# Optimization experiments

Hardware: AMD Instinct MI355X
Metric: run time of the kernel (lower is better)

## Reference

```python
import jax, jax.numpy as jnp
import numpy as np

L, B, D, Di, N, H, P, K, M, V = 4, 8, 2048, 4096, 128, 64, 64, 4, 8, 50288
Cch = Di + 2 * N           # conv channels = 4352
Dout = 2 * Di + 2 * N + H  # in_proj out = 8512
EPS = 1e-5


def _rms(x, w):
    return x * jax.lax.rsqrt(jnp.mean(x * x, axis=-1, keepdims=True) + EPS) * w


def setup_inputs() -> dict:
    key = jax.random.key(0)
    ks = jax.random.split(key, 16)
    s = 0.02
    return {
        "input_ids": jax.random.randint(ks[0], (B, 1), 0, V),
        "emb": jax.random.normal(ks[1], (V, D)) * s,
        "in_proj_w": jax.random.normal(ks[2], (L, D, Dout)) * s,
        "conv_w": jax.random.normal(ks[3], (L, Cch, K)) * s,
        "conv_b": jax.random.normal(ks[4], (L, Cch)) * s,
        "A_log": jax.random.normal(ks[5], (L, H)) * 0.5,
        "dt_bias": jax.random.normal(ks[6], (L, H)) * 0.5,
        "D_param": jax.random.normal(ks[7], (L, H)) * 0.5,
        "mixer_norm_w": jnp.ones((L, Di)),
        "out_proj_w": jax.random.normal(ks[8], (L, Di, D)) * s,
        "layer_norm_w": jnp.ones((L, D)),
        "norm_f_w": jnp.ones((D,)),
        "W_mc": jax.random.normal(ks[9], (L, M + 1)).at[:, -1].set(5.0),
        "conv_state": jax.random.normal(ks[10], (L, B, Cch, K)) * 0.1,
        "ssm_state": jax.random.normal(ks[11], (L, B, H, P, N)) * 0.1,
        "cached_states": jax.random.normal(ks[12], (L, B, M, H, P, N)) * 0.1,
    }


def reference(input_ids, emb, in_proj_w, conv_w, conv_b, A_log, dt_bias, D_param,
              mixer_norm_w, out_proj_w, layer_norm_w, norm_f_w, W_mc,
              conv_state, ssm_state, cached_states):
    ids = input_ids[:, 0]              # (B,)
    res = emb[ids]                     # (B, D) token embedding gather
    for l in range(L):
        xn = _rms(res, layer_norm_w[l])
        zxbcdt = xn @ in_proj_w[l]     # (B, Dout)
        z = zxbcdt[:, :Di]
        xBC = zxbcdt[:, Di:Di + Cch]
        dt = zxbcdt[:, Di + Cch:]
        # circular conv-state shift + depthwise conv over kernel dim
        cs = jnp.concatenate([conv_state[l][:, :, 1:], xBC[:, :, None]], axis=-1)
        xBC = jax.nn.silu(jnp.sum(cs * conv_w[l][None], axis=-1) + conv_b[l])
        x, Bm, Cm = xBC[:, :Di], xBC[:, Di:Di + N], xBC[:, Di + N:]
        dt = jax.nn.softplus(dt + dt_bias[l])                 # (B, H)
        dA = jnp.exp(dt * (-jnp.exp(A_log[l])))               # (B, H)
        x = x.reshape(B, H, P)
        dBx = jnp.einsum('bh,bn,bhp->bhpn', dt, Bm, x)        # (B,H,P,N)
        ssm = ssm_state[l] * dA[:, :, None, None] + dBx       # (B,H,P,N)
        # softmax-weighted fusion of cached segment states + current state
        w = jax.nn.softmax(W_mc[l])                           # (M+1,)
        fused = jnp.einsum('bmhpn,m->bhpn', cached_states[l], w[:-1]) + w[-1] * ssm
        y = jnp.einsum('bhpn,bn->bhp', fused, Cm) + D_param[l][None, :, None] * x
        y = y.reshape(B, Di)
        y = _rms(y * jax.nn.silu(z), mixer_norm_w[l])         # gated RMSNorm
        res = res + y @ out_proj_w[l]
    res = _rms(res, norm_f_w)
    logits = res @ emb.T               # tied lm_head
    return logits[:, None, :]          # (B, 1, V)
```

## Files before the change

### kernel.cpp

```cpp
#include <hip/hip_runtime.h>
#include <hip/hip_bf16.h>
#include <math.h>

#define LN 4
#define B_ 8
#define D_ 2048
#define DI 4096
#define N_ 128
#define H_ 64
#define P_ 64
#define K_ 4
#define M_ 8
#define V_ 50288
#define CCH (DI + 2*N_)
#define DOUT (2*DI + 2*N_ + H_)
#define EPSF 1e-5f
#define KT_IN 32
#define KT_OUT 128

typedef float f32x4 __attribute__((ext_vector_type(4)));

__device__ inline float wave_sum(float v) {
  #pragma unroll
  for (int off = 32; off > 0; off >>= 1) v += __shfl_xor(v, off, 64);
  return v;
}

__device__ inline float fold_reduce8(const float a[8], int lane) {
  float t0[4];
  #pragma unroll
  for (int r = 0; r < 4; ++r) {
    float keep = (lane & 1) ? a[2*r+1] : a[2*r];
    float send = (lane & 1) ? a[2*r]   : a[2*r+1];
    t0[r] = keep + __shfl_xor(send, 1, 64);
  }
  float t1[2];
  #pragma unroll
  for (int r = 0; r < 2; ++r) {
    float keep = (lane & 2) ? t0[2*r+1] : t0[2*r];
    float send = (lane & 2) ? t0[2*r]   : t0[2*r+1];
    t1[r] = keep + __shfl_xor(send, 2, 64);
  }
  float keep = (lane & 4) ? t1[1] : t1[0];
  float send = (lane & 4) ? t1[0] : t1[1];
  float u = keep + __shfl_xor(send, 4, 64);
  u += __shfl_xor(u, 8, 64);
  u += __shfl_xor(u, 16, 64);
  u += __shfl_xor(u, 32, 64);
  return u;
}

__global__ __launch_bounds__(256)
void k_rmsnorm(const float* __restrict__ in, const float* __restrict__ w,
               float* __restrict__ out) {
  __shared__ float lds[4];
  int b = blockIdx.x, tid = threadIdx.x;
  const float* row = in + (size_t)b * D_;
  f32x4 v0 = *reinterpret_cast<const f32x4*>(row + tid * 8);
  f32x4 v1 = *reinterpret_cast<const f32x4*>(row + tid * 8 + 4);
  float ss = v0[0]*v0[0] + v0[1]*v0[1] + v0[2]*v0[2] + v0[3]*v0[3]
           + v1[0]*v1[0] + v1[1]*v1[1] + v1[2]*v1[2] + v1[3]*v1[3];
  float wsum = wave_sum(ss);
  int lane = tid & 63, wid = tid >> 6;
  if (lane == 0) lds[wid] = wsum;
  __syncthreads();
  float tot = lds[0] + lds[1] + lds[2] + lds[3];
  float scale = rsqrtf(tot / (float)D_ + EPSF);
  f32x4 w0 = *reinterpret_cast<const f32x4*>(w + tid * 8);
  f32x4 w1 = *reinterpret_cast<const f32x4*>(w + tid * 8 + 4);
  f32x4 o0 = v0 * scale * w0, o1 = v1 * scale * w1;
  *reinterpret_cast<f32x4*>(out + (size_t)b * D_ + tid * 8)     = o0;
  *reinterpret_cast<f32x4*>(out + (size_t)b * D_ + tid * 8 + 4) = o1;
}

__global__ __launch_bounds__(256)
void k_inproj1(const float* __restrict__ res, const int* __restrict__ ids,
               const float* __restrict__ emb, const float* __restrict__ lnw,
               const float* __restrict__ W, float* __restrict__ pin) {
  __shared__ float xs[8][64];
  __shared__ float sred[4][8];
  int tid = threadIdx.x, lane = tid & 63, wid = tid >> 6;
  int jt = blockIdx.x % 9, kt = blockIdx.x / 9;
  int k0 = kt * 64;
  float ssq[8];
  #pragma unroll
  for (int r = 0; r < 8; ++r) {
    const float* row = ids ? (emb + (size_t)ids[r] * D_) : (res + (size_t)r * D_);
    f32x4 a = *reinterpret_cast<const f32x4*>(row + tid * 8);
    f32x4 c = *reinterpret_cast<const f32x4*>(row + tid * 8 + 4);
    ssq[r] = a[0]*a[0] + a[1]*a[1] + a[2]*a[2] + a[3]*a[3]
           + c[0]*c[0] + c[1]*c[1] + c[2]*c[2] + c[3]*c[3];
  }
  #pragma unroll
  for (int r = 0; r < 8; ++r) {
    float wsum = wave_sum(ssq[r]);
    if (lane == 0) sred[wid][r] = wsum;
  }
  __syncthreads();
  for (int i = tid; i < 8 * 64; i += 256) {
    int r = i >> 6, kk = i & 63;
    const float* row = ids ? (emb + (size_t)ids[r] * D_) : (res + (size_t)r * D_);
    float tot = sred[0][r] + sred[1][r] + sred[2][r] + sred[3][r];
    float scale = rsqrtf(tot / (float)D_ + EPSF);
    xs[r][kk] = row[k0 + kk] * scale * lnw[k0 + kk];
  }
  __syncthreads();
  int j = jt * 1024 + tid * 4;
  if (j >= DOUT) return;
  f32x4 acc[8];
  #pragma unroll
  for (int r = 0; r < 8; ++r) acc[r] = (f32x4)0.f;
  const float* Wp = W + (size_t)k0 * DOUT + j;
  for (int kk = 0; kk < 64; ++kk) {
    f32x4 w4 = __builtin_nontemporal_load(
        reinterpret_cast<const f32x4*>(Wp + (size_t)kk * DOUT));
    #pragma unroll
    for (int r = 0; r < 8; ++r) acc[r] += w4 * xs[r][kk];
  }
  #pragma unroll
  for (int r = 0; r < 8; ++r)
    *reinterpret_cast<f32x4*>(&pin[((size_t)kt * 8 + r) * DOUT + j]) = acc[r];
}

__global__ __launch_bounds__(256)
void k_inproj2_conv(const float* __restrict__ pin, const float* __restrict__ conv_state,
                    const float* __restrict__ conv_w, const float* __restrict__ conv_b,
                    const float* __restrict__ A_log, const float* __restrict__ dt_bias,
                    const float* __restrict__ W_mc,
                    float* __restrict__ zx, float* __restrict__ xbc,
                    float* __restrict__ dts, float* __restrict__ dav,
                    float* __restrict__ wmc) {
  const int TOT4 = B_ * DOUT / 4;
  int t = blockIdx.x * 256 + threadIdx.x;
  if (t >= TOT4) return;
  f32x4 s = (f32x4)0.f;
  const f32x4* p4 = reinterpret_cast<const f32x4*>(pin) + t;
  #pragma unroll 8
  for (int kt = 0; kt < KT_IN; ++kt) s += p4[(size_t)kt * TOT4];
  reinterpret_cast<f32x4*>(zx)[t] = s;
  int c4 = t * 4;
  int b = c4 / DOUT;
  int c = c4 - b * DOUT;
  #pragma unroll
  for (int e = 0; e < 4; ++e) {
    int ce = c + e;
    if (ce >= DI && ce < DI + CCH) {
      int cc = ce - DI;
      f32x4 cs4 = *reinterpret_cast<const f32x4*>(conv_state + ((size_t)b * CCH + cc) * K_);
      f32x4 cw4 = *reinterpret_cast<const f32x4*>(conv_w + (size_t)cc * K_);
      float v = cs4[1] * cw4[0] + cs4[2] * cw4[1] + cs4[3] * cw4[2]
              + s[e] * cw4[3] + conv_b[cc];
      xbc[b * CCH + cc] = v / (1.f + expf(-v));
    } else if (ce >= DI + CCH) {
      int h = ce - DI - CCH;
      float x = s[e] + dt_bias[h];
      float sp = (x > 20.f) ? x : log1pf(expf(x));
      dts[b * 64 + h] = sp;
      dav[b * 64 + h] = expf(-expf(A_log[h]) * sp);
    }
  }
  if (t == 0) {
    float mx = -1e30f;
    for (int i = 0; i < M_ + 1; ++i) mx = fmaxf(mx, W_mc[i]);
    float e2[M_ + 1], sum = 0.f;
    for (int i = 0; i < M_ + 1; ++i) { e2[i] = expf(W_mc[i] - mx); sum += e2[i]; }
    for (int i = 0; i < M_ + 1; ++i) wmc[i] = e2[i] / sum;
  }
}

__global__ __launch_bounds__(256)
void k_state(const float* __restrict__ xbc, const float* __restrict__ dts,
             const float* __restrict__ dav, const float* __restrict__ Dp_,
             const float* __restrict__ wmc, const float* __restrict__ ssm,
             const float* __restrict__ cached, float* __restrict__ y) {
  int wg = blockIdx.x * 4 + (threadIdx.x >> 6);
  int lane = threadIdx.x & 63;
  int b = wg >> 11;
  int h = (wg >> 5) & 63;
  int pp = wg & 31;
  int hf = lane >> 5, il = lane & 31;
  int p = pp * 2 + hf;
  float xv  = xbc[b * CCH + h * 64 + p];
  float dtv = dts[b * 64 + h];
  float da  = dav[b * 64 + h];
  float w8  = wmc[8];
  const f32x4* xb4 = reinterpret_cast<const f32x4*>(xbc);
  f32x4 B4 = xb4[b * (CCH / 4) + DI / 4 + il];
  f32x4 C4 = xb4[b * (CCH / 4) + DI / 4 + N_ / 4 + il];
  const f32x4* sp4 = reinterpret_cast<const f32x4*>(ssm) +
                     ((size_t)((b * H_ + h) * P_ + p)) * (N_ / 4) + il;
  const f32x4* cp4 = reinterpret_cast<const f32x4*>(cached) +
                     ((size_t)(((b * M_) * H_ + h) * P_ + p)) * (N_ / 4) + il;
  f32x4 s4 = __builtin_nontemporal_load(sp4);
  f32x4 f4 = (s4 * da + B4 * (dtv * xv)) * w8;
  #pragma unroll
  for (int m = 0; m < 8; ++m) {
    f32x4 c4 = __builtin_nontemporal_load(cp4 + (size_t)m * (H_ * P_ * N_ / 4));
    f4 += c4 * wmc[m];
  }
  f4 *= C4;
  float acc = f4[0] + f4[1] + f4[2] + f4[3];
  #pragma unroll
  for (int off = 1; off < 32; off <<= 1) acc += __shfl_xor(acc, off, 64);
  if (il == 0) y[b * DI + h * 64 + p] = acc + Dp_[h] * xv;
}

__global__ void k_gatednorm(const float* __restrict__ y, const float* __restrict__ zx,
                            const float* __restrict__ mnw, float* __restrict__ yg) {
  __shared__ float lds[8];
  int b = blockIdx.x;
  float tv[16];
  float ss = 0.f;
  #pragma unroll
  for (int t = 0; t < 16; ++t) {
    int i = threadIdx.x + t * 256;
    float z = zx[b * DOUT + i];
    float v = y[b * DI + i] * (z / (1.f + expf(-z)));
    tv[t] = v; ss += v * v;
  }
  float wsum = wave_sum(ss);
  int lane = threadIdx.x & 63, wid = threadIdx.x >> 6;
  if (lane == 0) lds[wid] = wsum;
  __syncthreads();
  float tot = lds[0] + lds[1] + lds[2] + lds[3];
  float scale = rsqrtf(tot / (float)DI + EPSF);
  #pragma unroll
  for (int t = 0; t < 16; ++t) {
    int i = threadIdx.x + t * 256;
    yg[b * DI + i] = tv[t] * scale * mnw[i];
  }
}

__global__ void k_outproj1(const float* __restrict__ yg, const float* __restrict__ W,
                           float* __restrict__ pout) {
  __shared__ float xs[8][32];
  int jt = blockIdx.x & 1, kt = blockIdx.x >> 1;
  int k0 = kt * 32;
  for (int i = threadIdx.x; i < 8 * 32; i += 256) {
    int r = i >> 5, kk = i & 31;
    xs[r][kk] = yg[r * DI + k0 + kk];
  }
  __syncthreads();
  int j = jt * 1024 + threadIdx.x * 4;
  f32x4 acc[8];
  #pragma unroll
  for (int r = 0; r < 8; ++r) acc[r] = (f32x4)0.f;
  const float* Wp = W + (size_t)k0 * D_ + j;
  for (int kk = 0; kk < 32; ++kk) {
    f32x4 w4 = __builtin_nontemporal_load(
        reinterpret_cast<const f32x4*>(Wp + (size_t)kk * D_));
    #pragma unroll
    for (int r = 0; r < 8; ++r) acc[r] += w4 * xs[r][kk];
  }
  #pragma unroll
  for (int r = 0; r < 8; ++r)
    *reinterpret_cast<f32x4*>(&pout[((size_t)kt * 8 + r) * D_ + j]) = acc[r];
}

__global__ __launch_bounds__(256)
void k_outproj2(const float* __restrict__ pout, float* __restrict__ res,
                const int* __restrict__ ids, const float* __restrict__ emb) {
  __shared__ f32x4 red[256];
  const int TOT4 = B_ * D_ / 4;
  int tid = threadIdx.x;
  int pos = blockIdx.x * 64 + (tid & 63);
  int kq = tid >> 6;
  const f32x4* p4 = reinterpret_cast<const f32x4*>(pout) + pos;
  f32x4 s = (f32x4)0.f;
  #pragma unroll 8
  for (int k = 0; k < 32; ++k)
    s += p4[(size_t)(kq * 32 + k) * TOT4];
  red[tid] = s;
  __syncthreads();
  if (tid < 64) {
    f32x4 tot = red[tid] + red[tid + 64] + red[tid + 128] + red[tid + 192];
    f32x4* r4 = reinterpret_cast<f32x4*>(res);
    if (ids) {
      int b = pos >> 9, d4 = pos & 511;
      f32x4 base = reinterpret_cast<const f32x4*>(emb)[(size_t)ids[b] * (D_ / 4) + d4];
      r4[pos] = base + tot;
    } else {
      r4[pos] += tot;
    }
  }
}

#define SL_ 4
#define KS_ (D_ / SL_)
#define NVB16 (V_ / 16)
__global__ __launch_bounds__(256)
void k_logits(const float* __restrict__ xn, const float* __restrict__ emb,
              float* __restrict__ pl) {
  __shared__ f32x4 xs[8][KS_ / 4];
  int s = blockIdx.x & 3, vb = blockIdx.x >> 2;
  const f32x4* xn4 = reinterpret_cast<const f32x4*>(xn);
  for (int i = threadIdx.x; i < 8 * (KS_ / 4); i += 256) {
    int r = i >> 7, q = i & 127;
    xs[r][q] = xn4[r * (D_ / 4) + s * (KS_ / 4) + q];
  }
  __syncthreads();
  int wid = threadIdx.x >> 6, lane = threadIdx.x & 63;
  int v0 = vb * 16 + wid * 4;
  const f32x4* e4 = reinterpret_cast<const f32x4*>(emb);
  #pragma unroll
  for (int vv = 0; vv < 4; ++vv) {
    int v = v0 + vv;
    const f32x4* ep = e4 + (size_t)v * (D_ / 4) + s * (KS_ / 4);
    float acc[8] = {0,0,0,0,0,0,0,0};
    #pragma unroll
    for (int st = 0; st < KS_ / 256; ++st) {
      int c = st * 64 + lane;
      f32x4 e = __builtin_nontemporal_load(ep + c);
      #pragma unroll
      for (int r = 0; r < 8; ++r) {
        f32x4 x = xs[r][c];
        acc[r] += e[0]*x[0] + e[1]*x[1] + e[2]*x[2] + e[3]*x[3];
      }
    }
    float u = fold_reduce8(acc, lane);
    if (lane < 8) pl[((size_t)s * 8 + lane) * V_ + v] = u;
  }
}

__global__ __launch_bounds__(256)
void k_logits2(const float* __restrict__ pl, float* __restrict__ out) {
  int v = blockIdx.x * 256 + threadIdx.x;
  if (v >= V_) return;
  int r = blockIdx.y;
  float t = pl[(size_t)r * V_ + v]
          + pl[((size_t)8  + r) * V_ + v]
          + pl[((size_t)16 + r) * V_ + v]
          + pl[((size_t)24 + r) * V_ + v];
  out[(size_t)r * V_ + v] = t;
}

extern "C" void kernel_launch(void* const* d_in, const int* in_sizes, int n_in,
                              void* d_out, int out_size, void* d_ws, size_t ws_size,
                              hipStream_t stream) {
  const int*   ids    = (const int*)  d_in[0];
  const float* emb    = (const float*)d_in[1];
  const float* inW    = (const float*)d_in[2];
  const float* convW  = (const float*)d_in[3];
  const float* convB  = (const float*)d_in[4];
  const float* Alog   = (const float*)d_in[5];
  const float* dtB    = (const float*)d_in[6];
  const float* Dpar   = (const float*)d_in[7];
  const float* mnw    = (const float*)d_in[8];
  const float* outW   = (const float*)d_in[9];
  const float* lnw    = (const float*)d_in[10];
  const float* nfw    = (const float*)d_in[11];
  const float* Wmc    = (const float*)d_in[12];
  const float* convS  = (const float*)d_in[13];
  const float* ssmS   = (const float*)d_in[14];
  const float* cached = (const float*)d_in[15];
  float* out = (float*)d_out;
  float* ws  = (float*)d_ws;

  float* res  = ws;
  float* xn   = ws + 16384;
  float* zx   = ws + 32768;
  float* xbc  = ws + 100864;
  float* dts  = ws + 135680;
  float* dav  = ws + 136192;
  float* wmc  = ws + 136704;
  float* y    = ws + 136768;
  float* yg   = ws + 169536;
  float* pin  = ws + 202304;
  float* pout = ws + 2381376;
  float* pl   = ws + 4478528;

  for (int l = 0; l < LN; ++l) {
    k_inproj1<<<288, 256, 0, stream>>>(res, (l == 0) ? ids : nullptr, emb,
                                       lnw + (size_t)l * D_,
                                       inW + (size_t)l * D_ * DOUT, pin);
    k_inproj2_conv<<<67, 256, 0, stream>>>(pin,
        convS + (size_t)l * B_ * CCH * K_, convW + (size_t)l * CCH * K_,
        convB + (size_t)l * CCH, Alog + l * H_, dtB + l * H_, Wmc + l * (M_ + 1),
        zx, xbc, dts, dav, wmc);
    k_state<<<4096, 256, 0, stream>>>(xbc, dts, dav, Dpar + l * H_, wmc,
        ssmS + (size_t)l * B_ * H_ * P_ * N_,
        cached + (size_t)l * B_ * M_ * H_ * P_ * N_, y);
    k_gatednorm<<<8, 256, 0, stream>>>(y, zx, mnw + (size_t)l * DI, yg);
    k_outproj1<<<256, 256, 0, stream>>>(yg, outW + (size_t)l * DI * D_, pout);
    k_outproj2<<<64, 256, 0, stream>>>(pout, res,
                                       (l == 0) ? ids : nullptr, emb);
  }
  k_rmsnorm<<<8, 256, 0, stream>>>(res, nfw, xn);
  k_logits<<<NVB16 * SL_, 256, 0, stream>>>(xn, emb, pl);
  k_logits2<<<dim3((V_ + 255) / 256, 8), 256, 0, stream>>>(pl, out);
}
```

Measured before the change: 435.5 us.

## Fuse RMS norm statistics into producer kernels via atomic sum-of-squares

Sum-of-squares statistics are now accumulated atomically by the kernels that produce each activation (outproj2 for the residual, k_state for the gated output). This removes the per-block recomputation of full-row norms in inproj1, and it drops the separate gated-norm and final rmsnorm kernels. inproj1 is also re-tiled to 320 threads covering 266 column quads per block, which removes the ragged-tail waste. The cost is float atomics, which make the reduction order nondeterministic, plus zero-initialisation that depends on kernel ordering.

```diff
diff --git a/kernel.cpp b/kernel.cpp
--- a/kernel.cpp
+++ b/kernel.cpp
@@ -17,6 +17,8 @@
 #define EPSF 1e-5f
 #define KT_IN 32
 #define KT_OUT 128
+#define NJ4 (DOUT / 4)
+#define JT_W 266
 
 typedef float f32x4 __attribute__((ext_vector_type(4)));
 
@@ -51,62 +53,40 @@
 }
 
 __global__ __launch_bounds__(256)
-void k_rmsnorm(const float* __restrict__ in, const float* __restrict__ w,
-               float* __restrict__ out) {
+void k_prenorm(const int* __restrict__ ids, const float* __restrict__ emb,
+               float* __restrict__ res, float* __restrict__ ssq_in) {
   __shared__ float lds[4];
   int b = blockIdx.x, tid = threadIdx.x;
-  const float* row = in + (size_t)b * D_;
+  const float* row = emb + (size_t)ids[b] * D_;
   f32x4 v0 = *reinterpret_cast<const f32x4*>(row + tid * 8);
   f32x4 v1 = *reinterpret_cast<const f32x4*>(row + tid * 8 + 4);
+  *reinterpret_cast<f32x4*>(res + (size_t)b * D_ + tid * 8)     = v0;
+  *reinterpret_cast<f32x4*>(res + (size_t)b * D_ + tid * 8 + 4) = v1;
   float ss = v0[0]*v0[0] + v0[1]*v0[1] + v0[2]*v0[2] + v0[3]*v0[3]
            + v1[0]*v1[0] + v1[1]*v1[1] + v1[2]*v1[2] + v1[3]*v1[3];
   float wsum = wave_sum(ss);
   int lane = tid & 63, wid = tid >> 6;
   if (lane == 0) lds[wid] = wsum;
   __syncthreads();
-  float tot = lds[0] + lds[1] + lds[2] + lds[3];
-  float scale = rsqrtf(tot / (float)D_ + EPSF);
-  f32x4 w0 = *reinterpret_cast<const f32x4*>(w + tid * 8);
-  f32x4 w1 = *reinterpret_cast<const f32x4*>(w + tid * 8 + 4);
-  f32x4 o0 = v0 * scale * w0, o1 = v1 * scale * w1;
-  *reinterpret_cast<f32x4*>(out + (size_t)b * D_ + tid * 8)     = o0;
-  *reinterpret_cast<f32x4*>(out + (size_t)b * D_ + tid * 8 + 4) = o1;
-}
-
-__global__ __launch_bounds__(256)
-void k_inproj1(const float* __restrict__ res, const int* __restrict__ ids,
-               const float* __restrict__ emb, const float* __restrict__ lnw,
-               const float* __restrict__ W, float* __restrict__ pin) {
+  if (tid == 0) ssq_in[b] = lds[0] + lds[1] + lds[2] + lds[3];
+}
+
+__global__ __launch_bounds__(320)
+void k_inproj1(const float* __restrict__ res, const float* __restrict__ ssq_in,
+               const float* __restrict__ lnw, const float* __restrict__ W,
+               float* __restrict__ pin) {
   __shared__ float xs[8][64];
-  __shared__ float sred[4][8];
-  int tid = threadIdx.x, lane = tid & 63, wid = tid >> 6;
-  int jt = blockIdx.x % 9, kt = blockIdx.x / 9;
+  int tid = threadIdx.x;
+  int jt = blockIdx.x >> 5, kt = blockIdx.x & 31;
   int k0 = kt * 64;
-  float ssq[8];
-  #pragma unroll
-  for (int r = 0; r < 8; ++r) {
-    const float* row = ids ? (emb + (size_t)ids[r] * D_) : (res + (size_t)r * D_);
-    f32x4 a = *reinterpret_cast<const f32x4*>(row + tid * 8);
-    f32x4 c = *reinterpret_cast<const f32x4*>(row + tid * 8 + 4);
-    ssq[r] = a[0]*a[0] + a[1]*a[1] + a[2]*a[2] + a[3]*a[3]
-           + c[0]*c[0] + c[1]*c[1] + c[2]*c[2] + c[3]*c[3];
-  }
-  #pragma unroll
-  for (int r = 0; r < 8; ++r) {
-    float wsum = wave_sum(ssq[r]);
-    if (lane == 0) sred[wid][r] = wsum;
-  }
-  __syncthreads();
-  for (int i = tid; i < 8 * 64; i += 256) {
+  for (int i = tid; i < 8 * 64; i += 320) {
     int r = i >> 6, kk = i & 63;
-    const float* row = ids ? (emb + (size_t)ids[r] * D_) : (res + (size_t)r * D_);
-    float tot = sred[0][r] + sred[1][r] + sred[2][r] + sred[3][r];
-    float scale = rsqrtf(tot / (float)D_ + EPSF);
-    xs[r][kk] = row[k0 + kk] * scale * lnw[k0 + kk];
-  }
-  __syncthreads();
-  int j = jt * 1024 + tid * 4;
-  if (j >= DOUT) return;
+    float scale = rsqrtf(ssq_in[r] / (float)D_ + EPSF);
+    xs[r][kk] = res[r * D_ + k0 + kk] * scale * lnw[k0 + kk];
+  }
+  __syncthreads();
+  if (tid >= JT_W) return;
+  int j = (jt * JT_W + tid) * 4;
   f32x4 acc[8];
   #pragma unroll
   for (int r = 0; r < 8; ++r) acc[r] = (f32x4)0.f;
@@ -129,7 +109,7 @@
                     const float* __restrict__ W_mc,
                     float* __restrict__ zx, float* __restrict__ xbc,
                     float* __restrict__ dts, float* __restrict__ dav,
-                    float* __restrict__ wmc) {
+                    float* __restrict__ wmc, float* __restrict__ gnorm_ssq) {
   const int TOT4 = B_ * DOUT / 4;
   int t = blockIdx.x * 256 + threadIdx.x;
   if (t >= TOT4) return;
@@ -165,14 +145,18 @@
     float e2[M_ + 1], sum = 0.f;
     for (int i = 0; i < M_ + 1; ++i) { e2[i] = expf(W_mc[i] - mx); sum += e2[i]; }
     for (int i = 0; i < M_ + 1; ++i) wmc[i] = e2[i] / sum;
-  }
-}
-
-__global__ __launch_bounds__(256)
-void k_state(const float* __restrict__ xbc, const float* __restrict__ dts,
-             const float* __restrict__ dav, const float* __restrict__ Dp_,
-             const float* __restrict__ wmc, const float* __restrict__ ssm,
-             const float* __restrict__ cached, float* __restrict__ y) {
+    #pragma unroll
+    for (int i = 0; i < 8; ++i) gnorm_ssq[i] = 0.f;
+  }
+}
+
+__global__ __launch_bounds__(256)
+void k_state(const float* __restrict__ xbc, const float* __restrict__ zx,
+             const float* __restrict__ dts, const float* __restrict__ dav,
+             const float* __restrict__ Dp_, const float* __restrict__ wmc,
+             const float* __restrict__ ssm, const float* __restrict__ cached,
+             float* __restrict__ y, float* __restrict__ gnorm_ssq) {
+  __shared__ float gred[8];
   int wg = blockIdx.x * 4 + (threadIdx.x >> 6);
   int lane = threadIdx.x & 63;
   int b = wg >> 11;
@@ -202,46 +186,41 @@
   float acc = f4[0] + f4[1] + f4[2] + f4[3];
   #pragma unroll
   for (int off = 1; off < 32; off <<= 1) acc += __shfl_xor(acc, off, 64);
-  if (il == 0) y[b * DI + h * 64 + p] = acc + Dp_[h] * xv;
-}
-
-__global__ void k_gatednorm(const float* __restrict__ y, const float* __restrict__ zx,
-                            const float* __restrict__ mnw, float* __restrict__ yg) {
-  __shared__ float lds[8];
-  int b = blockIdx.x;
-  float tv[16];
-  float ss = 0.f;
-  #pragma unroll
-  for (int t = 0; t < 16; ++t) {
-    int i = threadIdx.x + t * 256;
-    float z = zx[b * DOUT + i];
-    float v = y[b * DI + i] * (z / (1.f + expf(-z)));
-    tv[t] = v; ss += v * v;
-  }
-  float wsum = wave_sum(ss);
-  int lane = threadIdx.x & 63, wid = threadIdx.x >> 6;
-  if (lane == 0) lds[wid] = wsum;
-  __syncthreads();
-  float tot = lds[0] + lds[1] + lds[2] + lds[3];
-  float scale = rsqrtf(tot / (float)DI + EPSF);
-  #pragma unroll
-  for (int t = 0; t < 16; ++t) {
-    int i = threadIdx.x + t * 256;
-    yg[b * DI + i] = tv[t] * scale * mnw[i];
-  }
-}
-
-__global__ void k_outproj1(const float* __restrict__ yg, const float* __restrict__ W,
-                           float* __restrict__ pout) {
+  if (il == 0) {
+    float yv = acc + Dp_[h] * xv;
+    int d = h * 64 + p;
+    y[b * DI + d] = yv;
+    float z = zx[b * DOUT + d];
+    float v = yv * (z / (1.f + expf(-z)));
+    gred[(threadIdx.x >> 6) * 2 + hf] = v * v;
+  }
+  __syncthreads();
+  if (threadIdx.x == 0) {
+    float g = gred[0] + gred[1] + gred[2] + gred[3]
+            + gred[4] + gred[5] + gred[6] + gred[7];
+    atomicAdd(&gnorm_ssq[b], g);
+  }
+}
+
+__global__ __launch_bounds__(256)
+void k_outproj1(const float* __restrict__ y, const float* __restrict__ zx,
+                const float* __restrict__ mnw, const float* __restrict__ gnorm_ssq,
+                const float* __restrict__ W, float* __restrict__ pout,
+                float* __restrict__ ssq_in) {
   __shared__ float xs[8][32];
+  int tid = threadIdx.x;
+  if (blockIdx.x == 0 && tid < 8) ssq_in[tid] = 0.f;
   int jt = blockIdx.x & 1, kt = blockIdx.x >> 1;
   int k0 = kt * 32;
-  for (int i = threadIdx.x; i < 8 * 32; i += 256) {
-    int r = i >> 5, kk = i & 31;
-    xs[r][kk] = yg[r * DI + k0 + kk];
-  }
-  __syncthreads();
-  int j = jt * 1024 + threadIdx.x * 4;
+  {
+    int r = tid >> 5, kk = tid & 31;
+    float scale = rsqrtf(gnorm_ssq[r] / (float)DI + EPSF);
+    float z = zx[r * DOUT + k0 + kk];
+    float g = z / (1.f + expf(-z));
+    xs[r][kk] = y[r * DI + k0 + kk] * g * scale * mnw[k0 + kk];
+  }
+  __syncthreads();
+  int j = jt * 1024 + tid * 4;
   f32x4 acc[8];
   #pragma unroll
   for (int r = 0; r < 8; ++r) acc[r] = (f32x4)0.f;
@@ -259,7 +238,7 @@
 
 __global__ __launch_bounds__(256)
 void k_outproj2(const float* __restrict__ pout, float* __restrict__ res,
-                const int* __restrict__ ids, const float* __restrict__ emb) {
+                float* __restrict__ ssq_in) {
   __shared__ f32x4 red[256];
   const int TOT4 = B_ * D_ / 4;
   int tid = threadIdx.x;
@@ -275,13 +254,11 @@
   if (tid < 64) {
     f32x4 tot = red[tid] + red[tid + 64] + red[tid + 128] + red[tid + 192];
     f32x4* r4 = reinterpret_cast<f32x4*>(res);
-    if (ids) {
-      int b = pos >> 9, d4 = pos & 511;
-      f32x4 base = reinterpret_cast<const f32x4*>(emb)[(size_t)ids[b] * (D_ / 4) + d4];
-      r4[pos] = base + tot;
-    } else {
-      r4[pos] += tot;
-    }
+    f32x4 nv = r4[pos] + tot;
+    r4[pos] = nv;
+    float ps = nv[0]*nv[0] + nv[1]*nv[1] + nv[2]*nv[2] + nv[3]*nv[3];
+    ps = wave_sum(ps);
+    if (tid == 0) atomicAdd(&ssq_in[pos >> 9], ps);
   }
 }
 
@@ -289,14 +266,18 @@
 #define KS_ (D_ / SL_)
 #define NVB16 (V_ / 16)
 __global__ __launch_bounds__(256)
-void k_logits(const float* __restrict__ xn, const float* __restrict__ emb,
+void k_logits(const float* __restrict__ res, const float* __restrict__ ssq_in,
+              const float* __restrict__ nfw, const float* __restrict__ emb,
               float* __restrict__ pl) {
   __shared__ f32x4 xs[8][KS_ / 4];
   int s = blockIdx.x & 3, vb = blockIdx.x >> 2;
-  const f32x4* xn4 = reinterpret_cast<const f32x4*>(xn);
+  const f32x4* res4 = reinterpret_cast<const f32x4*>(res);
+  const f32x4* nfw4 = reinterpret_cast<const f32x4*>(nfw);
   for (int i = threadIdx.x; i < 8 * (KS_ / 4); i += 256) {
     int r = i >> 7, q = i & 127;
-    xs[r][q] = xn4[r * (D_ / 4) + s * (KS_ / 4) + q];
+    float scale = rsqrtf(ssq_in[r] / (float)D_ + EPSF);
+    xs[r][q] = res4[r * (D_ / 4) + s * (KS_ / 4) + q] * scale
+             * nfw4[s * (KS_ / 4) + q];
   }
   __syncthreads();
   int wid = threadIdx.x >> 6, lane = threadIdx.x & 63;
@@ -356,36 +337,34 @@
   float* out = (float*)d_out;
   float* ws  = (float*)d_ws;
 
-  float* res  = ws;
-  float* xn   = ws + 16384;
-  float* zx   = ws + 32768;
-  float* xbc  = ws + 100864;
-  float* dts  = ws + 135680;
-  float* dav  = ws + 136192;
-  float* wmc  = ws + 136704;
-  float* y    = ws + 136768;
-  float* yg   = ws + 169536;
-  float* pin  = ws + 202304;
-  float* pout = ws + 2381376;
-  float* pl   = ws + 4478528;
-
+  float* res   = ws;
+  float* zx    = ws + 16384;
+  float* xbc   = ws + 84480;
+  float* dts   = ws + 119296;
+  float* dav   = ws + 119808;
+  float* wmc   = ws + 120320;
+  float* ssqi  = ws + 120384;
+  float* gssq  = ws + 120448;
+  float* y     = ws + 120512;
+  float* pin   = ws + 153280;
+  float* pout  = ws + 2332352;
+  float* pl    = ws + 4429504;
+
+  k_prenorm<<<8, 256, 0, stream>>>(ids, emb, res, ssqi);
   for (int l = 0; l < LN; ++l) {
-    k_inproj1<<<288, 256, 0, stream>>>(res, (l == 0) ? ids : nullptr, emb,
-                                       lnw + (size_t)l * D_,
+    k_inproj1<<<256, 320, 0, stream>>>(res, ssqi, lnw + (size_t)l * D_,
                                        inW + (size_t)l * D_ * DOUT, pin);
     k_inproj2_conv<<<67, 256, 0, stream>>>(pin,
         convS + (size_t)l * B_ * CCH * K_, convW + (size_t)l * CCH * K_,
         convB + (size_t)l * CCH, Alog + l * H_, dtB + l * H_, Wmc + l * (M_ + 1),
-        zx, xbc, dts, dav, wmc);
-    k_state<<<4096, 256, 0, stream>>>(xbc, dts, dav, Dpar + l * H_, wmc,
+        zx, xbc, dts, dav, wmc, gssq);
+    k_state<<<4096, 256, 0, stream>>>(xbc, zx, dts, dav, Dpar + l * H_, wmc,
         ssmS + (size_t)l * B_ * H_ * P_ * N_,
-        cached + (size_t)l * B_ * M_ * H_ * P_ * N_, y);
-    k_gatednorm<<<8, 256, 0, stream>>>(y, zx, mnw + (size_t)l * DI, yg);
-    k_outproj1<<<256, 256, 0, stream>>>(yg, outW + (size_t)l * DI * D_, pout);
-    k_outproj2<<<64, 256, 0, stream>>>(pout, res,
-                                       (l == 0) ? ids : nullptr, emb);
-  }
-  k_rmsnorm<<<8, 256, 0, stream>>>(res, nfw, xn);
-  k_logits<<<NVB16 * SL_, 256, 0, stream>>>(xn, emb, pl);
+        cached + (size_t)l * B_ * M_ * H_ * P_ * N_, y, gssq);
+    k_outproj1<<<256, 256, 0, stream>>>(y, zx, mnw + (size_t)l * DI, gssq,
+                                        outW + (size_t)l * DI * D_, pout, ssqi);
+    k_outproj2<<<64, 256, 0, stream>>>(pout, res, ssqi);
+  }
+  k_logits<<<NVB16 * SL_, 256, 0, stream>>>(res, ssqi, nfw, emb, pl);
   k_logits2<<<dim3((V_ + 255) / 256, 8), 256, 0, stream>>>(pl, out);
 }
```

Result: slower. 547.9 us (+25.8%).
